# Optimization experiments

Measured on AMD Instinct MI355X. Metric: run time of the kernel, lower is better.

Reference implementation:

```python
import jax, jax.numpy as jnp
import numpy as np

# Model dims
B = 64            # scenes (memory batch)
APER = 16         # agents per scene (uniform `length`)
A = B * APER      # total agents = sum(length)
TPAST = 20
TFUT = 30         # len_future
C = 256           # controller_size
M = 128           # memory_m
N = 256           # memory_n
H = 5             # num_heads (future modes)
SPACE = N // APER # per-agent write slot band
EMB = 16
D = C + M         # decoder hidden size


def _gru(x, h, wih, whh, bih, bhh):
    """torch.nn.GRU single-cell step."""
    gi = x @ wih.T + bih
    gh = h @ whh.T + bhh
    ir, iz, inn = jnp.split(gi, 3, axis=-1)
    hr, hz, hn = jnp.split(gh, 3, axis=-1)
    r = jax.nn.sigmoid(ir + hr)
    z = jax.nn.sigmoid(iz + hz)
    n = jnp.tanh(inn + r * hn)
    return (1.0 - z) * n + z * h


def _address(k, beta, mem, mask):
    """NTM content addressing: beta-sharpened masked softmax over cosine sims.
    k: (...,B,APER,M), beta: (...,B,APER,1), mem: (B,N,M), mask: (APER,N)."""
    kn = k / (jnp.linalg.norm(k, axis=-1, keepdims=True) + 1e-16)
    mn = mem / (jnp.linalg.norm(mem, axis=-1, keepdims=True) + 1e-16)
    sim = jnp.einsum('...bam,bnm->...ban', kn, mn)
    logits = beta * sim + (mask - 1.0) * 1e9
    return jax.nn.softmax(logits, axis=-1)


def setup_inputs() -> dict:
    key = jax.random.key(0)
    ks = iter(jax.random.split(key, 64))
    def nrm(shape, scale):
        return jax.random.normal(next(ks), shape, dtype=jnp.float32) * scale
    inp = dict(
        past=nrm((A, TPAST, 2), 1.0),
        past_rel=nrm((A, TPAST, 2), 1.0),
        ep_w1=nrm((8, 2), 0.7), ep_b1=jnp.zeros(8), ep_w2=nrm((EMB, 8), 0.35), ep_b2=jnp.zeros(EMB),
        er_w1=nrm((8, 2), 0.7), er_b1=jnp.zeros(8), er_w2=nrm((EMB, 8), 0.35), er_b2=jnp.zeros(EMB),
        enc_wih=nrm((3 * C, EMB + M), 1.0 / np.sqrt(EMB + M)), enc_whh=nrm((3 * C, C), 1.0 / np.sqrt(C)),
        enc_bih=jnp.zeros(3 * C), enc_bhh=jnp.zeros(3 * C),
        rel_wih=nrm((3 * C, EMB), 1.0 / np.sqrt(EMB)), rel_whh=nrm((3 * C, C), 1.0 / np.sqrt(C)),
        rel_bih=jnp.zeros(3 * C), rel_bhh=jnp.zeros(3 * C),
        dec_wih=nrm((3 * D, D), 1.0 / np.sqrt(D)), dec_whh=nrm((3 * D, D), 1.0 / np.sqrt(D)),
        dec_bih=jnp.zeros(3 * D), dec_bhh=jnp.zeros(3 * D),
        out_w=nrm((2, D), 1.0 / np.sqrt(D)), out_b=jnp.zeros(2),
        read_w=nrm((H, M + 1, C), 1.0 / np.sqrt(C)), read_b=jnp.zeros((H, M + 1)),
        write_w=nrm((3 * M + 1, C), 1.0 / np.sqrt(C)), write_b=jnp.zeros(3 * M + 1),
        init_r=nrm((1, M), 0.01),
        h_bias=nrm((1, C), 0.05), h_rel_bias=nrm((1, C), 0.05), h_fut_bias=nrm((1, D), 0.05),
        mem_bias=nrm((N, M), 0.05),
    )
    return inp


def reference(past, past_rel, ep_w1, ep_b1, ep_w2, ep_b2, er_w1, er_b1, er_w2, er_b2,
              enc_wih, enc_whh, enc_bih, enc_bhh, rel_wih, rel_whh, rel_bih, rel_bhh,
              dec_wih, dec_whh, dec_bih, dec_bhh, out_w, out_b,
              read_w, read_b, write_w, write_b,
              init_r, h_bias, h_rel_bias, h_fut_bias, mem_bias):
    # Per-agent disjoint write bands; read mask = other agents' bands.
    owner = jnp.arange(N) // SPACE
    mask_w = (owner[None, :] == jnp.arange(APER)[:, None]).astype(jnp.float32)  # (APER,N)
    mask_r = 1.0 - mask_w

    def mlp(x, w1, b1, w2, b2):
        return jax.nn.relu(x @ w1.T + b1) @ w2.T + b2

    emb_p = jnp.transpose(mlp(past, ep_w1, ep_b1, ep_w2, ep_b2), (1, 0, 2))      # (T,A,16)
    emb_r = jnp.transpose(mlp(past_rel, er_w1, er_b1, er_w2, er_b2), (1, 0, 2))  # (T,A,16)

    def step(carry, xs):
        emb, embr = xs
        mem, h, hr, hf, r = carry
        h = _gru(jnp.concatenate([emb, r], axis=-1), h, enc_wih, enc_whh, enc_bih, enc_bhh)
        hr = _gru(embr, hr, rel_wih, rel_whh, rel_bih, rel_bhh)
        # write head: k, beta, erase, add
        wp = h @ write_w.T + write_b
        kw = jnp.tanh(wp[:, :M]).reshape(B, APER, M)
        betaw = jax.nn.softplus(wp[:, M:M + 1]).reshape(B, APER, 1)
        er = jax.nn.sigmoid(wp[:, M + 1:2 * M + 1]).reshape(B, APER, M)
        ad = jnp.tanh(wp[:, 2 * M + 1:]).reshape(B, APER, M)
        ww = _address(kw, betaw, mem, mask_w)                                    # (B,APER,N)
        # erase/add; write bands are disjoint across agents so aggregation is exact
        mem = mem * (1.0 - jnp.einsum('ban,bam->bnm', ww, er)) + jnp.einsum('ban,bam->bnm', ww, ad)
        # per-head reads
        rp = jnp.einsum('ac,hkc->hak', hr, read_w) + read_b[:, None, :]          # (H,A,M+1)
        kr = jnp.tanh(rp[..., :M]).reshape(H, B, APER, M)
        betar = jax.nn.softplus(rp[..., M:]).reshape(H, B, APER, 1)
        wr = _address(kr, betar, mem, mask_r)                                    # (H,B,APER,N)
        reads = jnp.einsum('hban,bnm->hbam', wr, mem).reshape(H, A, M)
        r = reads[0]
        # per-mode decoder
        dec_in = jnp.concatenate([jnp.broadcast_to(h[None], (H, A, C)), reads], axis=-1).reshape(H * A, D)
        hf = _gru(dec_in, hf, dec_wih, dec_whh, dec_bih, dec_bhh)
        out = (hf @ out_w.T + out_b).reshape(H, A, 2)
        return (mem, h, hr, hf, r), out

    carry0 = (jnp.broadcast_to(mem_bias[None], (B, N, M)),
              jnp.broadcast_to(h_bias, (A, C)),
              jnp.broadcast_to(h_rel_bias, (A, C)),
              jnp.broadcast_to(h_fut_bias, (H * A, D)),
              jnp.broadcast_to(init_r, (A, M)))
    carry, _ = jax.lax.scan(step, carry0, (emb_p, emb_r))
    zf = jnp.zeros((TFUT, A, EMB), dtype=past.dtype)
    carry, outs = jax.lax.scan(step, carry, (zf, zf))                            # (TFUT,H,A,2)
    pred_rel = jnp.transpose(outs, (2, 1, 0, 3))                                 # (A,H,TFUT,2)
    pred = past[:, -1][:, None, None, :] + jnp.cumsum(pred_rel, axis=2)
    return pred, pred_rel
```

## Files before the change

kernel.cpp:

```cpp
#include <hip/hip_runtime.h>
#include <math.h>

#define B_    64
#define APER_ 16
#define A_    1024
#define TPAST_ 20
#define TFUT_  30
#define C_    256
#define M_    128
#define N_    256
#define H_    5
#define EMB_  16
#define D_    384
#define TTOT_ 50

typedef short bf16x8 __attribute__((ext_vector_type(8)));
typedef float f32x4 __attribute__((ext_vector_type(4)));

__device__ __forceinline__ float sigmoidf_(float x) { return 1.0f / (1.0f + expf(-x)); }
__device__ __forceinline__ float softplusf_(float x) { return (x > 20.0f) ? x : log1pf(expf(x)); }
__device__ __forceinline__ unsigned short f2bf(float f) {
    unsigned u = __float_as_uint(f);
    return (unsigned short)((u + 0x7FFFu + ((u >> 16) & 1u)) >> 16);
}
__device__ __forceinline__ float bf2f(short s) {
    return __uint_as_float(((unsigned)(unsigned short)s) << 16);
}

struct Cvt { const float* src; short* dst; int rows, sk, dk, total; };
struct Cvt8 { Cvt c[8]; };

__global__ __launch_bounds__(256) void convert_all(Cvt8 p)
{
    const int stride = gridDim.x * 256;
    #pragma unroll
    for (int s = 0; s < 8; ++s) {
        const Cvt d = p.c[s];
        for (int idx = blockIdx.x * 256 + threadIdx.x; idx < d.total; idx += stride) {
            const int r = idx / d.dk, k = idx % d.dk;
            float v = (k < d.sk && r < d.rows) ? d.src[(size_t)r * d.sk + k] : 0.f;
            d.dst[idx] = (short)f2bf(v);
        }
    }
}

__global__ __launch_bounds__(256) void embed2_k(const float* __restrict__ past, const float* __restrict__ past_rel,
                                                const float* __restrict__ pw1, const float* __restrict__ pb1,
                                                const float* __restrict__ pw2, const float* __restrict__ pb2,
                                                const float* __restrict__ rw1, const float* __restrict__ rb1,
                                                const float* __restrict__ rw2, const float* __restrict__ rb2,
                                                short* __restrict__ emb_p, short* __restrict__ emb_r)
{
    const int idx0 = blockIdx.x * 256 + threadIdx.x;
    const int half = A_ * TPAST_;
    if (idx0 >= 2 * half) return;
    const bool second = idx0 >= half;
    const int idx = second ? idx0 - half : idx0;
    const float* x = second ? past_rel : past;
    const float* w1 = second ? rw1 : pw1; const float* b1 = second ? rb1 : pb1;
    const float* w2 = second ? rw2 : pw2; const float* b2 = second ? rb2 : pb2;
    short* emb = second ? emb_r : emb_p;

    const int a = idx / TPAST_, t = idx % TPAST_;
    const float x0 = x[(size_t)idx * 2], x1 = x[(size_t)idx * 2 + 1];
    float hbuf[8];
    #pragma unroll
    for (int j = 0; j < 8; ++j) hbuf[j] = fmaxf(0.f, w1[j * 2] * x0 + w1[j * 2 + 1] * x1 + b1[j]);
    short* e = emb + ((size_t)t * A_ + a) * EMB_;
    #pragma unroll
    for (int i = 0; i < 16; ++i) {
        float acc = b2[i];
        #pragma unroll
        for (int j = 0; j < 8; ++j) acc += w2[i * 8 + j] * hbuf[j];
        e[i] = (short)f2bf(acc);
    }
}

__global__ __launch_bounds__(256) void init_k(float* __restrict__ h, const float* __restrict__ h_bias, short* __restrict__ hb,
                                              float* __restrict__ hr, const float* __restrict__ hr_bias, short* __restrict__ hrb,
                                              const float* __restrict__ hf_bias, short* __restrict__ hfb,
                                              short* __restrict__ reads_b, const float* __restrict__ init_r,
                                              float* __restrict__ mem, short* __restrict__ memhi, short* __restrict__ memlo,
                                              float* __restrict__ normsG, const float* __restrict__ mem_bias)
{
    const int idx = blockIdx.x * 256 + threadIdx.x;
    if (idx < B_ * N_ * M_) {
        const float v = mem_bias[idx & (N_ * M_ - 1)];
        mem[idx] = v;
        const short hv = (short)f2bf(v);
        memhi[idx] = hv;
        memlo[idx] = (short)f2bf(v - bf2f(hv));
    }
    if (idx < B_ * N_) {
        const float* r = mem_bias + (size_t)(idx & (N_ - 1)) * M_;
        float ss = 0.f;
        for (int k = 0; k < M_; ++k) ss += r[k] * r[k];
        normsG[idx] = sqrtf(ss) + 1e-16f;
    }
    if (idx < A_ * C_) {
        float v = h_bias[idx & (C_ - 1)];
        h[idx] = v; hb[idx] = (short)f2bf(v);
        v = hr_bias[idx & (C_ - 1)];
        hr[idx] = v; hrb[idx] = (short)f2bf(v);
    }
    if (idx < H_ * A_ * D_) {
        hfb[idx] = (short)f2bf(hf_bias[idx % D_]);
    }
    if (idx < A_ * M_) reads_b[idx] = (short)f2bf(init_r[idx & (M_ - 1)]);
}

__device__ __forceinline__ void gru_tile(
    const short* __restrict__ X1, int K1,
    const short* __restrict__ X2, int K2,
    const short* __restrict__ Wih, int Kpad,
    const float* __restrict__ bih,
    const short* __restrict__ Hb, const short* __restrict__ Whh,
    const float* __restrict__ bhh,
    const float* __restrict__ Hprev,
    float* __restrict__ Hnew, short* __restrict__ Hnewb,
    int G, int rowBase, int colBase, int lane)
{
    const int l16 = lane & 15;
    const int kb8 = (lane >> 4) * 8;
    const f32x4 z4 = {0.f, 0.f, 0.f, 0.f};
    f32x4 ar[2][2], az[2][2], ani[2][2], anh[2][2];
    #pragma unroll
    for (int i = 0; i < 2; ++i)
        #pragma unroll
        for (int j = 0; j < 2; ++j) { ar[i][j] = z4; az[i][j] = z4; ani[i][j] = z4; anh[i][j] = z4; }

    const int kmax = (Kpad > G) ? Kpad : G;
    #pragma unroll 2
    for (int kc = 0; kc < kmax; kc += 32) {
        const int k8 = kc + kb8;
        if (kc < Kpad) {
            bf16x8 ax[2];
            #pragma unroll
            for (int i = 0; i < 2; ++i) {
                const int r = rowBase + i * 16 + l16;
                bf16x8 v = {0, 0, 0, 0, 0, 0, 0, 0};
                if (k8 < K1) {
                    if (X1) v = *(const bf16x8*)(X1 + (size_t)(r & 1023) * K1 + k8);
                } else if (k8 < K1 + K2) {
                    v = *(const bf16x8*)(X2 + (size_t)r * K2 + (k8 - K1));
                }
                ax[i] = v;
            }
            #pragma unroll
            for (int j = 0; j < 2; ++j) {
                const size_t wb = (size_t)(colBase + j * 16 + l16) * Kpad + k8;
                const bf16x8 b0 = *(const bf16x8*)(Wih + wb);
                const bf16x8 b1 = *(const bf16x8*)(Wih + (size_t)G * Kpad + wb);
                const bf16x8 b2 = *(const bf16x8*)(Wih + (size_t)2 * G * Kpad + wb);
                ar[0][j]  = __builtin_amdgcn_mfma_f32_16x16x32_bf16(ax[0], b0, ar[0][j], 0, 0, 0);
                ar[1][j]  = __builtin_amdgcn_mfma_f32_16x16x32_bf16(ax[1], b0, ar[1][j], 0, 0, 0);
                az[0][j]  = __builtin_amdgcn_mfma_f32_16x16x32_bf16(ax[0], b1, az[0][j], 0, 0, 0);
                az[1][j]  = __builtin_amdgcn_mfma_f32_16x16x32_bf16(ax[1], b1, az[1][j], 0, 0, 0);
                ani[0][j] = __builtin_amdgcn_mfma_f32_16x16x32_bf16(ax[0], b2, ani[0][j], 0, 0, 0);
                ani[1][j] = __builtin_amdgcn_mfma_f32_16x16x32_bf16(ax[1], b2, ani[1][j], 0, 0, 0);
            }
        }
        if (kc < G) {
            bf16x8 ah[2];
            #pragma unroll
            for (int i = 0; i < 2; ++i)
                ah[i] = *(const bf16x8*)(Hb + (size_t)(rowBase + i * 16 + l16) * G + k8);
            #pragma unroll
            for (int j = 0; j < 2; ++j) {
                const size_t wb = (size_t)(colBase + j * 16 + l16) * G + k8;
                const bf16x8 b0 = *(const bf16x8*)(Whh + wb);
                const bf16x8 b1 = *(const bf16x8*)(Whh + (size_t)G * G + wb);
                const bf16x8 b2 = *(const bf16x8*)(Whh + (size_t)2 * G * G + wb);
                ar[0][j]  = __builtin_amdgcn_mfma_f32_16x16x32_bf16(ah[0], b0, ar[0][j], 0, 0, 0);
                ar[1][j]  = __builtin_amdgcn_mfma_f32_16x16x32_bf16(ah[1], b0, ar[1][j], 0, 0, 0);
                az[0][j]  = __builtin_amdgcn_mfma_f32_16x16x32_bf16(ah[0], b1, az[0][j], 0, 0, 0);
                az[1][j]  = __builtin_amdgcn_mfma_f32_16x16x32_bf16(ah[1], b1, az[1][j], 0, 0, 0);
                anh[0][j] = __builtin_amdgcn_mfma_f32_16x16x32_bf16(ah[0], b2, anh[0][j], 0, 0, 0);
                anh[1][j] = __builtin_amdgcn_mfma_f32_16x16x32_bf16(ah[1], b2, anh[1][j], 0, 0, 0);
            }
        }
    }

    const int r4 = (lane >> 4) * 4;
    #pragma unroll
    for (int j = 0; j < 2; ++j) {
        const int col = colBase + j * 16 + l16;
        const float b0 = bih[col] + bhh[col];
        const float b1 = bih[G + col] + bhh[G + col];
        const float bi2 = bih[2 * G + col], bh2 = bhh[2 * G + col];
        #pragma unroll
        for (int i = 0; i < 2; ++i) {
            #pragma unroll
            for (int q = 0; q < 4; ++q) {
                const int row = rowBase + i * 16 + r4 + q;
                const float rr = sigmoidf_(ar[i][j][q] + b0);
                const float zz = sigmoidf_(az[i][j][q] + b1);
                const float nn = tanhf(ani[i][j][q] + bi2 + rr * (anh[i][j][q] + bh2));
                const float hp = Hprev ? Hprev[(size_t)row * G + col]
                                       : bf2f(Hb[(size_t)row * G + col]);
                const float hv = (1.f - zz) * nn + zz * hp;
                if (Hnew) Hnew[(size_t)row * G + col] = hv;
                Hnewb[(size_t)row * G + col] = (short)f2bf(hv);
            }
        }
    }
}

__device__ __forceinline__ void gemm_tile(
    const short* __restrict__ Xb, const short* __restrict__ Wb,
    const float* __restrict__ bias, float* __restrict__ Out,
    int Ncols, int K, int rowBase, int colBase, int lane)
{
    const int l16 = lane & 15;
    const int kb8 = (lane >> 4) * 8;
    const f32x4 z4 = {0.f, 0.f, 0.f, 0.f};
    f32x4 acc[2][2] = {{z4, z4}, {z4, z4}};

    for (int kc = 0; kc < K; kc += 32) {
        const int k8 = kc + kb8;
        const bf16x8 a0 = *(const bf16x8*)(Xb + (size_t)(rowBase + l16) * K + k8);
        const bf16x8 a1 = *(const bf16x8*)(Xb + (size_t)(rowBase + 16 + l16) * K + k8);
        const bf16x8 b0 = *(const bf16x8*)(Wb + (size_t)(colBase + l16) * K + k8);
        const bf16x8 b1 = *(const bf16x8*)(Wb + (size_t)(colBase + 16 + l16) * K + k8);
        acc[0][0] = __builtin_amdgcn_mfma_f32_16x16x32_bf16(a0, b0, acc[0][0], 0, 0, 0);
        acc[0][1] = __builtin_amdgcn_mfma_f32_16x16x32_bf16(a0, b1, acc[0][1], 0, 0, 0);
        acc[1][0] = __builtin_amdgcn_mfma_f32_16x16x32_bf16(a1, b0, acc[1][0], 0, 0, 0);
        acc[1][1] = __builtin_amdgcn_mfma_f32_16x16x32_bf16(a1, b1, acc[1][1], 0, 0, 0);
    }
    const int r4 = (lane >> 4) * 4;
    #pragma unroll
    for (int j = 0; j < 2; ++j) {
        const int col = colBase + j * 16 + l16;
        if (col >= Ncols) continue;
        const float bv = bias[col];
        #pragma unroll
        for (int i = 0; i < 2; ++i)
            #pragma unroll
            for (int q = 0; q < 4; ++q) {
                const int row = rowBase + i * 16 + r4 + q;
                Out[(size_t)row * Ncols + col] = acc[i][j][q] + bv;
            }
    }
}

__global__ __launch_bounds__(256) void phaseA(
    const short* __restrict__ ep, const short* __restrict__ er,
    const short* __restrict__ enc_wih, const float* __restrict__ enc_bih,
    const short* __restrict__ enc_whh, const float* __restrict__ enc_bhh,
    const short* __restrict__ rel_wih, const float* __restrict__ rel_bih,
    const short* __restrict__ rel_whh, const float* __restrict__ rel_bhh,
    const short* __restrict__ dec_wih, const float* __restrict__ dec_bih,
    const short* __restrict__ dec_whh, const float* __restrict__ dec_bhh,
    const float* __restrict__ hc, const short* __restrict__ hbc,
    float* __restrict__ hn, short* __restrict__ hbn,
    const float* __restrict__ hrc, const short* __restrict__ hrbc,
    float* __restrict__ hrn, short* __restrict__ hrbn,
    const short* __restrict__ hfbc, short* __restrict__ hfbn,
    const short* __restrict__ reads_b,
    int decBlocks, int encBlocks)
{
    const int bid = blockIdx.x;
    const int wave = threadIdx.x >> 6;
    const int lane = threadIdx.x & 63;

    if (bid < decBlocks) {
        const int tile = bid * 4 + wave;
        gru_tile(hbc, 256, reads_b, 128, dec_wih, 384, dec_bih,
                 hfbc, dec_whh, dec_bhh, nullptr, nullptr, hfbn, D_,
                 (tile / 12) * 32, (tile % 12) * 32, lane);
    } else if (bid < decBlocks + encBlocks) {
        const int tile = (bid - decBlocks) * 4 + wave;
        gru_tile(ep, 16, reads_b, 128, enc_wih, 160, enc_bih,
                 hbc, enc_whh, enc_bhh, hc, hn, hbn, C_,
                 (tile >> 3) * 32, (tile & 7) * 32, lane);
    } else {
        const int tile = (bid - decBlocks - encBlocks) * 4 + wave;
        gru_tile(er, 16, nullptr, 0, rel_wih, 32, rel_bih,
                 hrbc, rel_whh, rel_bhh, hrc, hrn, hrbn, C_,
                 (tile >> 3) * 32, (tile & 7) * 32, lane);
    }
}

__global__ __launch_bounds__(256) void phaseHeads(
    const short* __restrict__ hbn, const short* __restrict__ write_w_b,
    const float* __restrict__ write_b, float* __restrict__ wp,
    const short* __restrict__ hrbn, const short* __restrict__ read_w_b,
    const float* __restrict__ read_b, float* __restrict__ rp,
    const short* __restrict__ hfbn, const float* __restrict__ out_w,
    const float* __restrict__ out_b, float* __restrict__ predrel,
    int outT, int wpBlocks, int rpBlocks)
{
    const int bid = blockIdx.x;
    const int wave = threadIdx.x >> 6;
    const int lane = threadIdx.x & 63;

    if (bid < wpBlocks) {
        const int tile = bid * 4 + wave;
        gemm_tile(hbn, write_w_b, write_b, wp, 385, C_,
                  (tile & 31) * 32, (tile >> 5) * 32, lane);
    } else if (bid < wpBlocks + rpBlocks) {
        const int tile = (bid - wpBlocks) * 4 + wave;
        gemm_tile(hrbn, read_w_b, read_b, rp, 645, C_,
                  (tile & 31) * 32, (tile >> 5) * 32, lane);
    } else {
        const int widx = (bid - wpBlocks - rpBlocks) * 4 + wave;
        const int g = lane >> 3, li = lane & 7;
        const int row = widx * 8 + g;
        const short* hrow = hfbn + (size_t)row * D_;
        float a0 = 0.f, a1 = 0.f;
        #pragma unroll
        for (int u = 0; u < 6; ++u) {
            const int k0 = u * 64 + li * 8;
            const bf16x8 v = *(const bf16x8*)(hrow + k0);
            #pragma unroll
            for (int r = 0; r < 8; ++r) {
                const float f = bf2f(v[r]);
                a0 = fmaf(f, out_w[k0 + r], a0);
                a1 = fmaf(f, out_w[D_ + k0 + r], a1);
            }
        }
        a0 += __shfl_xor(a0, 1); a0 += __shfl_xor(a0, 2); a0 += __shfl_xor(a0, 4);
        a1 += __shfl_xor(a1, 1); a1 += __shfl_xor(a1, 2); a1 += __shfl_xor(a1, 4);
        if (li == 0) {
            const int hh = row >> 10, aa = row & 1023;
            float* o = predrel + (((size_t)aa * H_ + hh) * TFUT_ + outT) * 2;
            o[0] = a0 + out_b[0];
            o[1] = a1 + out_b[1];
        }
    }
}

__global__ __launch_bounds__(256) void write_mem_k(const float* __restrict__ wp,
                                                   float* __restrict__ mem,
                                                   short* __restrict__ memhi, short* __restrict__ memlo,
                                                   float* __restrict__ normsG)
{
    const int a = blockIdx.x;
    const int b = a >> 4, p = a & 15;
    __shared__ float kw[128], er[128], ad[128], red[256], ww[16], logit[16];
    __shared__ float buf[2048];
    __shared__ float beta_s, knorm_s;
    const int tid = threadIdx.x;
    const float* w = wp + (size_t)a * 385;
    if (tid < 128) {
        kw[tid] = tanhf(w[tid]);
        er[tid] = sigmoidf_(w[129 + tid]);
        ad[tid] = tanhf(w[257 + tid]);
    }
    if (tid == 0) beta_s = softplusf_(w[128]);
    __syncthreads();

    red[tid] = (tid < 128) ? kw[tid] * kw[tid] : 0.f;
    __syncthreads();
    for (int s = 128; s > 0; s >>= 1) { if (tid < s) red[tid] += red[tid + s]; __syncthreads(); }
    if (tid == 0) knorm_s = sqrtf(red[0]) + 1e-16f;
    __syncthreads();

    const int s = tid >> 4, j = tid & 15;
    float dot = 0.f, ss = 0.f;
    {
        const float* mrow = mem + ((size_t)(b * N_) + p * 16 + s) * M_;
        for (int k = j; k < 128; k += 16) { float v = mrow[k]; dot += kw[k] * v; ss += v * v; }
    }
    red[tid] = dot; __syncthreads();
    for (int st = 8; st > 0; st >>= 1) { if (j < st) red[tid] += red[tid + st]; __syncthreads(); }
    float dotf = red[s * 16];
    __syncthreads();
    red[tid] = ss; __syncthreads();
    for (int st = 8; st > 0; st >>= 1) { if (j < st) red[tid] += red[tid + st]; __syncthreads(); }
    float ssf = red[s * 16];
    if (j == 0) {
        float mn = sqrtf(ssf) + 1e-16f;
        logit[s] = beta_s * (dotf / (mn * knorm_s));
    }
    __syncthreads();
    if (tid == 0) {
        float mx = -1e30f;
        for (int i = 0; i < 16; ++i) mx = fmaxf(mx, logit[i]);
        float sum = 0.f;
        for (int i = 0; i < 16; ++i) { float e = __expf(logit[i] - mx); ww[i] = e; sum += e; }
        float inv = 1.f / sum;
        for (int i = 0; i < 16; ++i) ww[i] *= inv;
    }
    __syncthreads();
    for (int idx = tid; idx < 16 * 128; idx += 256) {
        int si = idx >> 7, m = idx & 127;
        size_t g = ((size_t)(b * N_) + p * 16 + si) * M_ + m;
        float wwv = ww[si];
        float v = mem[g] * (1.f - wwv * er[m]) + wwv * ad[m];
        mem[g] = v;
        const short hv = (short)f2bf(v);
        memhi[g] = hv;
        memlo[g] = (short)f2bf(v - bf2f(hv));
        buf[idx] = v;
    }
    __syncthreads();
    {
        float ssq = 0.f;
        #pragma unroll
        for (int i = 0; i < 8; ++i) { float v = buf[s * 128 + j + 16 * i]; ssq += v * v; }
        #pragma unroll
        for (int m = 1; m < 16; m <<= 1) ssq += __shfl_xor(ssq, m);
        if (j == 0) normsG[b * N_ + p * 16 + s] = sqrtf(ssq) + 1e-16f;
    }
}

__global__ __launch_bounds__(256) void read_k2(const float* __restrict__ rp,
                                               const float* __restrict__ mem,
                                               const short* __restrict__ memhi,
                                               const short* __restrict__ memlo,
                                               const float* __restrict__ normsG,
                                               short* __restrict__ reads_b)
{
    const int b = blockIdx.x;
    const int h = blockIdx.y;
    __shared__ __align__(16) float kq[16 * 132];
    __shared__ float S[16 * 260];
    __shared__ float beta_s[16], knorm_s[16], inv_s[16];
    const int t = threadIdx.x;
    const int a = t >> 4;
    const int sub = t & 15;

    {
        const float* base = rp + ((size_t)(b * 16 + a)) * 645 + h * 129;
        const int k0 = sub * 8;
        float v[8]; float ss = 0.f;
        #pragma unroll
        for (int r = 0; r < 8; ++r) { v[r] = tanhf(base[k0 + r]); ss += v[r] * v[r]; }
        float* dst = kq + a * 132 + k0;
        *(float4*)dst = make_float4(v[0], v[1], v[2], v[3]);
        *(float4*)(dst + 4) = make_float4(v[4], v[5], v[6], v[7]);
        #pragma unroll
        for (int m = 1; m < 16; m <<= 1) ss += __shfl_xor(ss, m);
        if (sub == 0) {
            knorm_s[a] = sqrtf(ss) + 1e-16f;
            beta_s[a] = softplusf_(base[128]);
        }
    }
    __syncthreads();

    {
        const int wave = t >> 6, lane = t & 63;
        const int l16 = lane & 15, kb8 = (lane >> 4) * 8;
        const int slotBase = wave * 64;
        const f32x4 z4 = {0.f, 0.f, 0.f, 0.f};
        f32x4 acc[4] = {z4, z4, z4, z4};
        const short* mbh = memhi + (size_t)b * N_ * M_;
        const short* mbl = memlo + (size_t)b * N_ * M_;
        #pragma unroll
        for (int kc = 0; kc < 128; kc += 32) {
            const float* ap = kq + l16 * 132 + kc + kb8;
            bf16x8 ah, al;
            #pragma unroll
            for (int r = 0; r < 8; ++r) {
                const float av = ap[r];
                const short hv = (short)f2bf(av);
                ah[r] = hv; al[r] = (short)f2bf(av - bf2f(hv));
            }
            #pragma unroll
            for (int tt = 0; tt < 4; ++tt) {
                const size_t roff = (size_t)(slotBase + tt * 16 + l16) * M_ + kc + kb8;
                const bf16x8 bh = *(const bf16x8*)(mbh + roff);
                const bf16x8 bl = *(const bf16x8*)(mbl + roff);
                acc[tt] = __builtin_amdgcn_mfma_f32_16x16x32_bf16(ah, bh, acc[tt], 0, 0, 0);
                acc[tt] = __builtin_amdgcn_mfma_f32_16x16x32_bf16(ah, bl, acc[tt], 0, 0, 0);
                acc[tt] = __builtin_amdgcn_mfma_f32_16x16x32_bf16(al, bh, acc[tt], 0, 0, 0);
            }
        }
        const int r4 = (lane >> 4) * 4;
        #pragma unroll
        for (int tt = 0; tt < 4; ++tt) {
            const int slot = slotBase + tt * 16 + l16;
            const float nv = normsG[b * N_ + slot];
            #pragma unroll
            for (int q = 0; q < 4; ++q) {
                const int aq = r4 + q;
                const float lg = ((slot >> 4) == aq) ? -1e30f
                               : beta_s[aq] * acc[tt][q] / (nv * knorm_s[aq]);
                S[aq * 260 + slot] = lg;
            }
        }
    }
    __syncthreads();

    {
        float mx = -1e30f;
        #pragma unroll
        for (int i = 0; i < 16; ++i) mx = fmaxf(mx, S[a * 260 + sub + 16 * i]);
        #pragma unroll
        for (int m = 1; m < 16; m <<= 1) mx = fmaxf(mx, __shfl_xor(mx, m));
        float e[16]; float sum = 0.f;
        #pragma unroll
        for (int i = 0; i < 16; ++i) { e[i] = __expf(S[a * 260 + sub + 16 * i] - mx); sum += e[i]; }
        #pragma unroll
        for (int i = 0; i < 16; ++i) S[a * 260 + sub + 16 * i] = e[i];
        #pragma unroll
        for (int m = 1; m < 16; m <<= 1) sum += __shfl_xor(sum, m);
        if (sub == 0) inv_s[a] = 1.f / sum;
    }
    __syncthreads();

    {
        const int m0 = sub * 8;
        const float* mb = mem + (size_t)b * N_ * M_ + m0;
        float acc[8];
        #pragma unroll
        for (int r = 0; r < 8; ++r) acc[r] = 0.f;
        const float* Sa = S + a * 260;
        #pragma unroll 4
        for (int n = 0; n < N_; ++n) {
            const float w = Sa[n];
            const float4 v0 = *(const float4*)(mb + (size_t)n * M_);
            const float4 v1 = *(const float4*)(mb + (size_t)n * M_ + 4);
            acc[0] = fmaf(w, v0.x, acc[0]); acc[1] = fmaf(w, v0.y, acc[1]);
            acc[2] = fmaf(w, v0.z, acc[2]); acc[3] = fmaf(w, v0.w, acc[3]);
            acc[4] = fmaf(w, v1.x, acc[4]); acc[5] = fmaf(w, v1.y, acc[5]);
            acc[6] = fmaf(w, v1.z, acc[6]); acc[7] = fmaf(w, v1.w, acc[7]);
        }
        const float inv = inv_s[a];
        short pk[8];
        #pragma unroll
        for (int r = 0; r < 8; ++r) pk[r] = (short)f2bf(acc[r] * inv);
        *(bf16x8*)(reads_b + ((size_t)h * A_ + b * 16 + a) * M_ + m0) = *(bf16x8*)pk;
    }
}

__global__ __launch_bounds__(256) void cumsum_k(const float* __restrict__ past,
                                                const float* __restrict__ predrel,
                                                float* __restrict__ pred)
{
    const int idx = blockIdx.x * 256 + threadIdx.x;
    if (idx >= A_ * H_ * 2) return;
    const int c = idx & 1;
    const int ah = idx >> 1;
    const int a = ah / H_;
    float acc = past[((size_t)a * TPAST_ + TPAST_ - 1) * 2 + c];
    const float* pr = predrel + (size_t)ah * TFUT_ * 2 + c;
    float* pd = pred + (size_t)ah * TFUT_ * 2 + c;
    for (int t = 0; t < TFUT_; ++t) { acc += pr[t * 2]; pd[t * 2] = acc; }
}

extern "C" void kernel_launch(void* const* d_in, const int* in_sizes, int n_in,
                              void* d_out, int out_size, void* d_ws, size_t ws_size,
                              hipStream_t stream)
{
    const float* past       = (const float*)d_in[0];
    const float* past_rel   = (const float*)d_in[1];
    const float* ep_w1      = (const float*)d_in[2];
    const float* ep_b1      = (const float*)d_in[3];
    const float* ep_w2      = (const float*)d_in[4];
    const float* ep_b2      = (const float*)d_in[5];
    const float* er_w1      = (const float*)d_in[6];
    const float* er_b1      = (const float*)d_in[7];
    const float* er_w2      = (const float*)d_in[8];
    const float* er_b2      = (const float*)d_in[9];
    const float* enc_wih    = (const float*)d_in[10];
    const float* enc_whh    = (const float*)d_in[11];
    const float* enc_bih    = (const float*)d_in[12];
    const float* enc_bhh    = (const float*)d_in[13];
    const float* rel_wih    = (const float*)d_in[14];
    const float* rel_whh    = (const float*)d_in[15];
    const float* rel_bih    = (const float*)d_in[16];
    const float* rel_bhh    = (const float*)d_in[17];
    const float* dec_wih    = (const float*)d_in[18];
    const float* dec_whh    = (const float*)d_in[19];
    const float* dec_bih    = (const float*)d_in[20];
    const float* dec_bhh    = (const float*)d_in[21];
    const float* out_w      = (const float*)d_in[22];
    const float* out_b      = (const float*)d_in[23];
    const float* read_w     = (const float*)d_in[24];
    const float* read_b     = (const float*)d_in[25];
    const float* write_w    = (const float*)d_in[26];
    const float* write_b    = (const float*)d_in[27];
    const float* init_r     = (const float*)d_in[28];
    const float* h_bias     = (const float*)d_in[29];
    const float* h_rel_bias = (const float*)d_in[30];
    const float* h_fut_bias = (const float*)d_in[31];
    const float* mem_bias   = (const float*)d_in[32];

    float* pred    = (float*)d_out;
    float* predrel = pred + (size_t)A_ * H_ * TFUT_ * 2;

    float* ws = (float*)d_ws;
    size_t off = 0;
    auto alloc = [&](size_t n) { float* p = ws + off; off += n; return p; };
    float* h0     = alloc((size_t)A_ * C_);
    float* h1     = alloc((size_t)A_ * C_);
    float* hr0    = alloc((size_t)A_ * C_);
    float* hr1    = alloc((size_t)A_ * C_);
    float* mem    = alloc((size_t)B_ * N_ * M_);
    float* wp     = alloc((size_t)A_ * 385);
    float* rp     = alloc((size_t)A_ * 645);
    float* normsG = alloc((size_t)B_ * N_);

    short* sws = (short*)(ws + off);
    size_t soff = 0;
    auto salloc = [&](size_t n) { short* p = sws + soff; soff += n; return p; };
    short* emb_p_b   = salloc((size_t)TPAST_ * A_ * EMB_);
    short* emb_r_b   = salloc((size_t)TPAST_ * A_ * EMB_);
    short* hb0       = salloc((size_t)A_ * C_);
    short* hb1       = salloc((size_t)A_ * C_);
    short* hrb0      = salloc((size_t)A_ * C_);
    short* hrb1      = salloc((size_t)A_ * C_);
    short* hfb0      = salloc((size_t)H_ * A_ * D_);
    short* hfb1      = salloc((size_t)H_ * A_ * D_);
    short* reads_b   = salloc((size_t)H_ * A_ * M_);
    short* memhi     = salloc((size_t)B_ * N_ * M_);
    short* memlo     = salloc((size_t)B_ * N_ * M_);
    short* enc_wih_b = salloc((size_t)768 * 160);
    short* enc_whh_b = salloc((size_t)768 * 256);
    short* rel_wih_b = salloc((size_t)768 * 32);
    short* rel_whh_b = salloc((size_t)768 * 256);
    short* dec_wih_b = salloc((size_t)1152 * 384);
    short* dec_whh_b = salloc((size_t)1152 * 384);
    short* write_w_b = salloc((size_t)416 * 256);
    short* read_w_b  = salloc((size_t)672 * 256);
    (void)ws_size; (void)in_sizes; (void)n_in; (void)out_size;

    Cvt8 cp;
    cp.c[0] = {enc_wih, enc_wih_b, 768, 144, 160, 768 * 160};
    cp.c[1] = {enc_whh, enc_whh_b, 768, 256, 256, 768 * 256};
    cp.c[2] = {rel_wih, rel_wih_b, 768, 16, 32, 768 * 32};
    cp.c[3] = {rel_whh, rel_whh_b, 768, 256, 256, 768 * 256};
    cp.c[4] = {dec_wih, dec_wih_b, 1152, 384, 384, 1152 * 384};
    cp.c[5] = {dec_whh, dec_whh_b, 1152, 384, 384, 1152 * 384};
    cp.c[6] = {write_w, write_w_b, 385, 256, 256, 416 * 256};
    cp.c[7] = {read_w, read_w_b, 645, 256, 256, 672 * 256};
    convert_all<<<1024, 256, 0, stream>>>(cp);

    init_k<<<(B_ * N_ * M_ + 255) / 256, 256, 0, stream>>>(
        h0, h_bias, hb0, hr0, h_rel_bias, hrb0, h_fut_bias, hfb0,
        reads_b, init_r, mem, memhi, memlo, normsG, mem_bias);
    embed2_k<<<(2 * A_ * TPAST_ + 255) / 256, 256, 0, stream>>>(
        past, past_rel, ep_w1, ep_b1, ep_w2, ep_b2, er_w1, er_b1, er_w2, er_b2,
        emb_p_b, emb_r_b);

    float *hc = h0, *hn = h1, *hrc = hr0, *hrn = hr1;
    short *hbc = hb0, *hbn = hb1, *hrbc = hrb0, *hrbn = hrb1, *hfbc = hfb0, *hfbn = hfb1;

    const dim3 g_read(B_, H_);

    for (int t = 0; t < TTOT_; ++t) {
        const short* ep = (t < TPAST_) ? emb_p_b + (size_t)t * A_ * EMB_ : nullptr;
        const short* er = (t < TPAST_) ? emb_r_b + (size_t)t * A_ * EMB_ : nullptr;

        const int decBlocks = (t == 0) ? 0 : 480;
        phaseA<<<decBlocks + 128, 256, 0, stream>>>(
            ep, er,
            enc_wih_b, enc_bih, enc_whh_b, enc_bhh,
            rel_wih_b, rel_bih, rel_whh_b, rel_bhh,
            dec_wih_b, dec_bih, dec_whh_b, dec_bhh,
            hc, hbc, hn, hbn,
            hrc, hrbc, hrn, hrbn,
            hfbc, hfbn,
            reads_b, decBlocks, 64);

        const int gridH = (t >= 21) ? 432 : 272;
        phaseHeads<<<gridH, 256, 0, stream>>>(
            hbn, write_w_b, write_b, wp,
            hrbn, read_w_b, read_b, rp,
            hfbn, out_w, out_b, predrel, t - 21, 104, 168);

        write_mem_k<<<A_, 256, 0, stream>>>(wp, mem, memhi, memlo, normsG);

        read_k2<<<g_read, 256, 0, stream>>>(rp, mem, memhi, memlo, normsG, reads_b);

        float* tf; short* ts;
        tf = hc; hc = hn; hn = tf;       ts = hbc; hbc = hbn; hbn = ts;
        tf = hrc; hrc = hrn; hrn = tf;   ts = hrbc; hrbc = hrbn; hrbn = ts;
        if (t >= 1) {
            ts = hfbc; hfbc = hfbn; hfbn = ts;
        }
    }

    phaseA<<<480, 256, 0, stream>>>(
        nullptr, nullptr,
        enc_wih_b, enc_bih, enc_whh_b, enc_bhh,
        rel_wih_b, rel_bih, rel_whh_b, rel_bhh,
        dec_wih_b, dec_bih, dec_whh_b, dec_bhh,
        hc, hbc, hn, hbn,
        hrc, hrbc, hrn, hrbn,
        hfbc, hfbn,
        reads_b, 480, 0);
    phaseHeads<<<160, 256, 0, stream>>>(
        hbn, write_w_b, write_b, wp,
        hrbn, read_w_b, read_b, rp,
        hfbn, out_w, out_b, predrel, TFUT_ - 1, 0, 0);
    cumsum_k<<<(A_ * H_ * 2 + 255) / 256, 256, 0, stream>>>(past, predrel, pred);
}
```

Baseline: 6.413 ms.

## Split GRU tile K-reduction across wave pairs with LDS exchange

Each GRU output tile is now computed by two waves: one accumulates the input-to-hidden products and the other the hidden-to-hidden products. The first wave writes its partial gate sums to shared memory, and after a block barrier the second wave combines them and applies the gate nonlinearities. The grid size doubles so that per-wave serial K-loop length and per-wave latency drop. In exchange it adds shared-memory traffic, a __syncthreads, and extra blocks. The unroll-by-2 pragma on the K loop is also dropped.

```diff
diff --git a/kernel.cpp b/kernel.cpp
--- a/kernel.cpp
+++ b/kernel.cpp
@@ -109,7 +109,8 @@
     if (idx < A_ * M_) reads_b[idx] = (short)f2bf(init_r[idx & (M_ - 1)]);
 }
 
-__device__ __forceinline__ void gru_tile(
+__device__ __forceinline__ void gru_tile_split(
+    int role, float* __restrict__ xchLane,
     const short* __restrict__ X1, int K1,
     const short* __restrict__ X2, int K2,
     const short* __restrict__ Wih, int Kpad,
@@ -123,17 +124,15 @@
     const int l16 = lane & 15;
     const int kb8 = (lane >> 4) * 8;
     const f32x4 z4 = {0.f, 0.f, 0.f, 0.f};
-    f32x4 ar[2][2], az[2][2], ani[2][2], anh[2][2];
+    f32x4 a0[2][2], a1[2][2], a2[2][2];
     #pragma unroll
     for (int i = 0; i < 2; ++i)
         #pragma unroll
-        for (int j = 0; j < 2; ++j) { ar[i][j] = z4; az[i][j] = z4; ani[i][j] = z4; anh[i][j] = z4; }
-
-    const int kmax = (Kpad > G) ? Kpad : G;
-    #pragma unroll 2
-    for (int kc = 0; kc < kmax; kc += 32) {
-        const int k8 = kc + kb8;
-        if (kc < Kpad) {
+        for (int j = 0; j < 2; ++j) { a0[i][j] = z4; a1[i][j] = z4; a2[i][j] = z4; }
+
+    if (role == 0) {
+        for (int kc = 0; kc < Kpad; kc += 32) {
+            const int k8 = kc + kb8;
             bf16x8 ax[2];
             #pragma unroll
             for (int i = 0; i < 2; ++i) {
@@ -152,15 +151,28 @@
                 const bf16x8 b0 = *(const bf16x8*)(Wih + wb);
                 const bf16x8 b1 = *(const bf16x8*)(Wih + (size_t)G * Kpad + wb);
                 const bf16x8 b2 = *(const bf16x8*)(Wih + (size_t)2 * G * Kpad + wb);
-                ar[0][j]  = __builtin_amdgcn_mfma_f32_16x16x32_bf16(ax[0], b0, ar[0][j], 0, 0, 0);
-                ar[1][j]  = __builtin_amdgcn_mfma_f32_16x16x32_bf16(ax[1], b0, ar[1][j], 0, 0, 0);
-                az[0][j]  = __builtin_amdgcn_mfma_f32_16x16x32_bf16(ax[0], b1, az[0][j], 0, 0, 0);
-                az[1][j]  = __builtin_amdgcn_mfma_f32_16x16x32_bf16(ax[1], b1, az[1][j], 0, 0, 0);
-                ani[0][j] = __builtin_amdgcn_mfma_f32_16x16x32_bf16(ax[0], b2, ani[0][j], 0, 0, 0);
-                ani[1][j] = __builtin_amdgcn_mfma_f32_16x16x32_bf16(ax[1], b2, ani[1][j], 0, 0, 0);
-            }
-        }
-        if (kc < G) {
+                a0[0][j] = __builtin_amdgcn_mfma_f32_16x16x32_bf16(ax[0], b0, a0[0][j], 0, 0, 0);
+                a0[1][j] = __builtin_amdgcn_mfma_f32_16x16x32_bf16(ax[1], b0, a0[1][j], 0, 0, 0);
+                a1[0][j] = __builtin_amdgcn_mfma_f32_16x16x32_bf16(ax[0], b1, a1[0][j], 0, 0, 0);
+                a1[1][j] = __builtin_amdgcn_mfma_f32_16x16x32_bf16(ax[1], b1, a1[1][j], 0, 0, 0);
+                a2[0][j] = __builtin_amdgcn_mfma_f32_16x16x32_bf16(ax[0], b2, a2[0][j], 0, 0, 0);
+                a2[1][j] = __builtin_amdgcn_mfma_f32_16x16x32_bf16(ax[1], b2, a2[1][j], 0, 0, 0);
+            }
+        }
+        #pragma unroll
+        for (int i = 0; i < 2; ++i)
+            #pragma unroll
+            for (int j = 0; j < 2; ++j)
+                #pragma unroll
+                for (int q = 0; q < 4; ++q) {
+                    const int base = (i * 2 + j) * 4 + q;
+                    xchLane[base]      = a0[i][j][q];
+                    xchLane[16 + base] = a1[i][j][q];
+                    xchLane[32 + base] = a2[i][j][q];
+                }
+    } else {
+        for (int kc = 0; kc < G; kc += 32) {
+            const int k8 = kc + kb8;
             bf16x8 ah[2];
             #pragma unroll
             for (int i = 0; i < 2; ++i)
@@ -171,31 +183,38 @@
                 const bf16x8 b0 = *(const bf16x8*)(Whh + wb);
                 const bf16x8 b1 = *(const bf16x8*)(Whh + (size_t)G * G + wb);
                 const bf16x8 b2 = *(const bf16x8*)(Whh + (size_t)2 * G * G + wb);
-                ar[0][j]  = __builtin_amdgcn_mfma_f32_16x16x32_bf16(ah[0], b0, ar[0][j], 0, 0, 0);
-                ar[1][j]  = __builtin_amdgcn_mfma_f32_16x16x32_bf16(ah[1], b0, ar[1][j], 0, 0, 0);
-                az[0][j]  = __builtin_amdgcn_mfma_f32_16x16x32_bf16(ah[0], b1, az[0][j], 0, 0, 0);
-                az[1][j]  = __builtin_amdgcn_mfma_f32_16x16x32_bf16(ah[1], b1, az[1][j], 0, 0, 0);
-                anh[0][j] = __builtin_amdgcn_mfma_f32_16x16x32_bf16(ah[0], b2, anh[0][j], 0, 0, 0);
-                anh[1][j] = __builtin_amdgcn_mfma_f32_16x16x32_bf16(ah[1], b2, anh[1][j], 0, 0, 0);
-            }
-        }
-    }
+                a0[0][j] = __builtin_amdgcn_mfma_f32_16x16x32_bf16(ah[0], b0, a0[0][j], 0, 0, 0);
+                a0[1][j] = __builtin_amdgcn_mfma_f32_16x16x32_bf16(ah[1], b0, a0[1][j], 0, 0, 0);
+                a1[0][j] = __builtin_amdgcn_mfma_f32_16x16x32_bf16(ah[0], b1, a1[0][j], 0, 0, 0);
+                a1[1][j] = __builtin_amdgcn_mfma_f32_16x16x32_bf16(ah[1], b1, a1[1][j], 0, 0, 0);
+                a2[0][j] = __builtin_amdgcn_mfma_f32_16x16x32_bf16(ah[0], b2, a2[0][j], 0, 0, 0);
+                a2[1][j] = __builtin_amdgcn_mfma_f32_16x16x32_bf16(ah[1], b2, a2[1][j], 0, 0, 0);
+            }
+        }
+    }
+    __syncthreads();
+    if (role != 1) return;
 
     const int r4 = (lane >> 4) * 4;
     #pragma unroll
     for (int j = 0; j < 2; ++j) {
         const int col = colBase + j * 16 + l16;
-        const float b0 = bih[col] + bhh[col];
-        const float b1 = bih[G + col] + bhh[G + col];
+        const float b0c = bih[col] + bhh[col];
+        const float b1c = bih[G + col] + bhh[G + col];
         const float bi2 = bih[2 * G + col], bh2 = bhh[2 * G + col];
         #pragma unroll
         for (int i = 0; i < 2; ++i) {
             #pragma unroll
             for (int q = 0; q < 4; ++q) {
                 const int row = rowBase + i * 16 + r4 + q;
-                const float rr = sigmoidf_(ar[i][j][q] + b0);
-                const float zz = sigmoidf_(az[i][j][q] + b1);
-                const float nn = tanhf(ani[i][j][q] + bi2 + rr * (anh[i][j][q] + bh2));
+                const int base = (i * 2 + j) * 4 + q;
+                const float arv = a0[i][j][q] + xchLane[base];
+                const float azv = a1[i][j][q] + xchLane[16 + base];
+                const float aniv = xchLane[32 + base];
+                const float anhv = a2[i][j][q];
+                const float rr = sigmoidf_(arv + b0c);
+                const float zz = sigmoidf_(azv + b1c);
+                const float nn = tanhf(aniv + bi2 + rr * (anhv + bh2));
                 const float hp = Hprev ? Hprev[(size_t)row * G + col]
                                        : bf2f(Hb[(size_t)row * G + col]);
                 const float hv = (1.f - zz) * nn + zz * hp;
@@ -259,25 +278,31 @@
     const short* __restrict__ reads_b,
     int decBlocks, int encBlocks)
 {
+    __shared__ float xch[2][64][49];
     const int bid = blockIdx.x;
-    const int wave = threadIdx.x >> 6;
+    const int wv = threadIdx.x >> 6;
     const int lane = threadIdx.x & 63;
+    const int pair = wv >> 1, role = wv & 1;
+    float* xchLane = &xch[pair][lane][0];
 
     if (bid < decBlocks) {
-        const int tile = bid * 4 + wave;
-        gru_tile(hbc, 256, reads_b, 128, dec_wih, 384, dec_bih,
-                 hfbc, dec_whh, dec_bhh, nullptr, nullptr, hfbn, D_,
-                 (tile / 12) * 32, (tile % 12) * 32, lane);
+        const int tile = bid * 2 + pair;
+        gru_tile_split(role, xchLane,
+                       hbc, 256, reads_b, 128, dec_wih, 384, dec_bih,
+                       hfbc, dec_whh, dec_bhh, nullptr, nullptr, hfbn, D_,
+                       (tile / 12) * 32, (tile % 12) * 32, lane);
     } else if (bid < decBlocks + encBlocks) {
-        const int tile = (bid - decBlocks) * 4 + wave;
-        gru_tile(ep, 16, reads_b, 128, enc_wih, 160, enc_bih,
-                 hbc, enc_whh, enc_bhh, hc, hn, hbn, C_,
-                 (tile >> 3) * 32, (tile & 7) * 32, lane);
+        const int tile = (bid - decBlocks) * 2 + pair;
+        gru_tile_split(role, xchLane,
+                       ep, 16, reads_b, 128, enc_wih, 160, enc_bih,
+                       hbc, enc_whh, enc_bhh, hc, hn, hbn, C_,
+                       (tile >> 3) * 32, (tile & 7) * 32, lane);
     } else {
-        const int tile = (bid - decBlocks - encBlocks) * 4 + wave;
-        gru_tile(er, 16, nullptr, 0, rel_wih, 32, rel_bih,
-                 hrbc, rel_whh, rel_bhh, hrc, hrn, hrbn, C_,
-                 (tile >> 3) * 32, (tile & 7) * 32, lane);
+        const int tile = (bid - decBlocks - encBlocks) * 2 + pair;
+        gru_tile_split(role, xchLane,
+                       er, 16, nullptr, 0, rel_wih, 32, rel_bih,
+                       hrbc, rel_whh, rel_bhh, hrc, hrn, hrbn, C_,
+                       (tile >> 3) * 32, (tile & 7) * 32, lane);
     }
 }
 
@@ -644,8 +669,8 @@
         const short* ep = (t < TPAST_) ? emb_p_b + (size_t)t * A_ * EMB_ : nullptr;
         const short* er = (t < TPAST_) ? emb_r_b + (size_t)t * A_ * EMB_ : nullptr;
 
-        const int decBlocks = (t == 0) ? 0 : 480;
-        phaseA<<<decBlocks + 128, 256, 0, stream>>>(
+        const int decBlocks = (t == 0) ? 0 : 960;
+        phaseA<<<decBlocks + 256, 256, 0, stream>>>(
             ep, er,
             enc_wih_b, enc_bih, enc_whh_b, enc_bhh,
             rel_wih_b, rel_bih, rel_whh_b, rel_bhh,
@@ -653,7 +678,7 @@
             hc, hbc, hn, hbn,
             hrc, hrbc, hrn, hrbn,
             hfbc, hfbn,
-            reads_b, decBlocks, 64);
+            reads_b, decBlocks, 128);
 
         const int gridH = (t >= 21) ? 432 : 272;
         phaseHeads<<<gridH, 256, 0, stream>>>(
@@ -673,7 +698,7 @@
         }
     }
 
-    phaseA<<<480, 256, 0, stream>>>(
+    phaseA<<<960, 256, 0, stream>>>(
         nullptr, nullptr,
         enc_wih_b, enc_bih, enc_whh_b, enc_bhh,
         rel_wih_b, rel_bih, rel_whh_b, rel_bhh,
@@ -681,7 +706,7 @@
         hc, hbc, hn, hbn,
         hrc, hrbc, hrn, hrbn,
         hfbc, hfbn,
-        reads_b, 480, 0);
+        reads_b, 960, 0);
     phaseHeads<<<160, 256, 0, stream>>>(
         hbn, write_w_b, write_b, wp,
         hrbn, read_w_b, read_b, rp,
```

Result: faster. 6.146 ms (-4.2%).
